# Optimization experiments

Measured on AMD Instinct MI355X. Metric: run time of the kernel, lower is better.

Reference implementation:

```python
import jax, jax.numpy as jnp
import numpy as np

DIM_IN, DIM_Q, DIM_K = 1024, 128, 128
B, S = 8, 2048

def setup_inputs() -> dict:
    key = jax.random.key(0)
    ks = jax.random.split(key, 9)
    sq = 1.0 / np.sqrt(DIM_IN)
    return {
        "query": jax.random.normal(ks[0], (B, S, DIM_IN), jnp.float32),
        "key": jax.random.normal(ks[1], (B, S, DIM_IN), jnp.float32),
        "value": jax.random.normal(ks[2], (B, S, DIM_IN), jnp.float32),
        "Wq": jax.random.uniform(ks[3], (DIM_IN, DIM_Q), jnp.float32, -sq, sq),
        "bq": jax.random.uniform(ks[4], (DIM_Q,), jnp.float32, -sq, sq),
        "Wk": jax.random.uniform(ks[5], (DIM_IN, DIM_K), jnp.float32, -sq, sq),
        "bk": jax.random.uniform(ks[6], (DIM_K,), jnp.float32, -sq, sq),
        "Wv": jax.random.uniform(ks[7], (DIM_IN, DIM_K), jnp.float32, -sq, sq),
        "bv": jax.random.uniform(ks[8], (DIM_K,), jnp.float32, -sq, sq),
    }

def reference(query, key, value, Wq, bq, Wk, bk, Wv, bv):
    q = jnp.einsum("bsd,dq->bsq", query, Wq) + bq          # [B,S,Dq]
    k = jnp.einsum("bsd,dk->bsk", key, Wk) + bk            # [B,S,Dk]
    v = jnp.einsum("bsd,dk->bsk", value, Wv) + bv          # [B,S,Dk]
    scale = jnp.asarray(q.shape[-1] ** 0.5, q.dtype)
    scores = jnp.einsum("bqd,bkd->bqk", q, k) / scale      # [B,S,S]
    attn = jax.nn.softmax(scores, axis=-1)
    return jnp.einsum("bqk,bkd->bqd", attn, v)             # [B,S,Dk]
```

## Files before the change

kernel.cpp:

```cpp
#include <hip/hip_runtime.h>

typedef __attribute__((ext_vector_type(8))) short short8;
typedef __attribute__((ext_vector_type(4))) float floatx4;

#define MFMA16(a, b, c) __builtin_amdgcn_mfma_f32_16x16x32_bf16(a, b, c, 0, 0, 0)

__device__ __forceinline__ short f2bf(float f) {
    unsigned int u = __float_as_uint(f);
    u = u + 0x7fffu + ((u >> 16) & 1u);
    return (short)(u >> 16);
}

__device__ __forceinline__ void ldst16(const void* g, void* l) {
    __builtin_amdgcn_global_load_lds(
        (const __attribute__((address_space(1))) void*)g,
        (__attribute__((address_space(3))) void*)l, 16, 0, 0);
}

__global__ __launch_bounds__(256) void wconv_kernel(const float* __restrict__ Wq,
                                                    const float* __restrict__ Wk,
                                                    const float* __restrict__ Wv,
                                                    short* __restrict__ wtf) {
    int idx = blockIdx.x * 256 + threadIdx.x;
    int w = idx >> 17;
    int rem = idx & 131071;
    int ks = rem >> 12;
    int r2 = rem & 4095;
    int nt = r2 >> 9;
    int r3 = r2 & 511;
    int lane = r3 >> 3, e = r3 & 7;
    int q4 = lane >> 4, l16 = lane & 15;
    int n = 16 * nt + l16;
    int k = 32 * ks + 8 * q4 + e;
    const float* W = (w == 0) ? Wq : (w == 1) ? Wk : Wv;
    wtf[idx] = f2bf(W[k * 128 + n]);
}

__global__ __launch_bounds__(256, 3) void proj_kernel(const float* __restrict__ Q,
                                                      const float* __restrict__ K,
                                                      const float* __restrict__ V,
                                                      const short* __restrict__ wtf,
                                                      const float* __restrict__ bq,
                                                      const float* __restrict__ bk,
                                                      const float* __restrict__ bv,
                                                      short* __restrict__ qo,
                                                      short* __restrict__ ko,
                                                      short* __restrict__ vo) {
    alignas(16) __shared__ float Asl[2][64 * 64];
    const int t = threadIdx.x;
    const int wv = t >> 6, L = t & 63;
    const int wm = wv >> 1, wn = wv & 1;
    const int q4 = L >> 4, l16 = L & 15;
    const int which = blockIdx.y;
    const float* A = (which == 0) ? Q : (which == 1) ? K : V;
    const short* Wf = wtf + which * 131072;
    const float* bias = (which == 0) ? bq : (which == 1) ? bk : bv;
    const int m0 = blockIdx.x * 64;

    floatx4 acc[2][4];
#pragma unroll
    for (int rg = 0; rg < 2; rg++)
#pragma unroll
        for (int nt = 0; nt < 4; nt++) acc[rg][nt] = (floatx4)0.0f;

    auto stage = [&](int buf, int k0) {
#pragma unroll
        for (int j = 0; j < 4; j++) {
            int s = j * 256 + t;
            int r = s >> 4, c = (s & 15) ^ (r & 15);
            ldst16(A + (size_t)(m0 + r) * 1024 + k0 + (c << 2),
                   &Asl[buf][(j * 256 + 64 * wv) * 4]);
        }
    };

    auto loadB = [&](int kc, short8 (&dst)[2][4]) {
#pragma unroll
        for (int ks = 0; ks < 2; ks++)
#pragma unroll
            for (int nt = 0; nt < 4; nt++)
                dst[ks][nt] = *(const short8*)(Wf +
                    (((size_t)(2 * kc + ks) * 8 + 4 * wn + nt) * 64 + L) * 8);
    };

    auto computeC = [&](int kc, short8 (&bfr)[2][4]) {
        short8 af[2][2];
#pragma unroll
        for (int rg = 0; rg < 2; rg++)
#pragma unroll
            for (int ks = 0; ks < 2; ks++) {
                int r = 32 * wm + 16 * rg + l16;
                int c0 = 8 * ks + 2 * q4;
                float4 f0 = *(float4*)&Asl[kc & 1][(r * 16 + (c0 ^ l16)) * 4];
                float4 f1 = *(float4*)&Asl[kc & 1][(r * 16 + ((c0 + 1) ^ l16)) * 4];
                short8 v;
                v[0] = f2bf(f0.x); v[1] = f2bf(f0.y); v[2] = f2bf(f0.z); v[3] = f2bf(f0.w);
                v[4] = f2bf(f1.x); v[5] = f2bf(f1.y); v[6] = f2bf(f1.z); v[7] = f2bf(f1.w);
                af[rg][ks] = v;
            }
        __builtin_amdgcn_s_setprio(1);
#pragma unroll
        for (int ks = 0; ks < 2; ks++)
#pragma unroll
            for (int nt = 0; nt < 4; nt++) {
                acc[0][nt] = MFMA16(af[0][ks], bfr[ks][nt], acc[0][nt]);
                acc[1][nt] = MFMA16(af[1][ks], bfr[ks][nt], acc[1][nt]);
            }
        __builtin_amdgcn_s_setprio(0);
    };

    short8 bA[2][4], bB[2][4];

#define PROJ_STEP(KC, BUSE, BLOAD)                                          \
    {                                                                       \
        if ((KC) + 1 < 16) {                                                \
            stage(((KC) + 1) & 1, ((KC) + 1) * 64);                         \
            loadB((KC) + 1, BLOAD);                                         \
            asm volatile("s_waitcnt vmcnt(12)" ::: "memory");               \
        } else {                                                            \
            asm volatile("s_waitcnt vmcnt(0)" ::: "memory");                \
        }                                                                   \
        __builtin_amdgcn_s_barrier();                                       \
        __builtin_amdgcn_sched_barrier(0);                                  \
        computeC((KC), BUSE);                                               \
        __builtin_amdgcn_sched_barrier(0);                                  \
        __builtin_amdgcn_s_barrier();                                       \
    }

    stage(0, 0);
    loadB(0, bA);

    for (int kc = 0; kc < 16; kc += 2) {
        PROJ_STEP(kc, bA, bB);
        PROJ_STEP(kc + 1, bB, bA);
    }
#undef PROJ_STEP

#pragma unroll
    for (int rg = 0; rg < 2; rg++) {
        const int rbase = m0 + 32 * wm + 16 * rg + q4 * 4;
#pragma unroll
        for (int nt = 0; nt < 4; nt++) {
            const int col = 64 * wn + 16 * nt + l16;
            float bvv = bias[col];
#pragma unroll
            for (int r = 0; r < 4; r++) {
                short h = f2bf(acc[rg][nt][r] + bvv);
                int grow = rbase + r;
                if (which == 0) {
                    qo[(size_t)grow * 128 + col] = h;
                } else if (which == 1) {
                    ko[(size_t)grow * 128 + col] = h;
                } else {
                    int bb = grow >> 11, s = grow & 2047;
                    vo[(size_t)bb * 262144 + (size_t)col * 2048 + s] = h;
                }
            }
        }
    }
}

__global__ __launch_bounds__(512, 2) void flash_kernel(const short* __restrict__ qw,
                                                       const short* __restrict__ kw,
                                                       const short* __restrict__ vw,
                                                       float* __restrict__ out) {
    alignas(16) __shared__ short Kls[2][2][64 * 128];
    alignas(16) __shared__ short Vls[2][2][128 * 64];
    alignas(16) __shared__ short Pl[2][64][72];
    const int t = threadIdx.x;
    const int wvi = t >> 6, L = t & 63;
    const int pr = wvi >> 2, wq = wvi & 3;
    const int pt = t & 255;
    const int q4 = L >> 4, l16 = L & 15;
    const int bid = blockIdx.x;
    const int b = bid & 7, bq = bid >> 3;
    const short* qp = qw + (size_t)b * 262144 + (size_t)bq * 64 * 128;
    const short* kp = kw + (size_t)b * 262144;
    const short* vp = vw + (size_t)b * 262144;

    short8 qf[4];
#pragma unroll
    for (int ks = 0; ks < 4; ks++)
        qf[ks] = *(const short8*)(qp + (16 * wq + l16) * 128 + ks * 32 + q4 * 8);

    floatx4 oacc[8];
#pragma unroll
    for (int dt = 0; dt < 8; dt++) oacc[dt] = (floatx4)0.0f;
    float ps[4] = {0.f, 0.f, 0.f, 0.f};
    const float SL = (float)(0.08838834764831845 * 1.4426950408889634);

    auto stage = [&](int buf, int kt) {
        const int kv0 = pr * 1024 + kt * 64;
#pragma unroll
        for (int j = 0; j < 4; j++) {
            int s = j * 256 + pt;
            int r = s >> 4, c = (s & 15) ^ (r & 15);
            ldst16(kp + (size_t)(kv0 + r) * 128 + c * 8,
                   &Kls[buf][pr][(j * 256 + 64 * wq) * 8]);
        }
#pragma unroll
        for (int j = 0; j < 4; j++) {
            int s = j * 256 + pt;
            int r = s >> 3, c = (s & 7) ^ (r & 7);
            ldst16(vp + (size_t)r * 2048 + kv0 + c * 8,
                   &Vls[buf][pr][(j * 256 + 64 * wq) * 8]);
        }
    };

    stage(0, 0);

    int cur = 0;
    for (int kt = 0; kt < 16; kt++) {
        if (kt + 1 < 16) {
            stage(cur ^ 1, kt + 1);
            asm volatile("s_waitcnt vmcnt(8)" ::: "memory");
        } else {
            asm volatile("s_waitcnt vmcnt(0)" ::: "memory");
        }
        __builtin_amdgcn_s_barrier();
        __builtin_amdgcn_sched_barrier(0);

        floatx4 sa[4];
        __builtin_amdgcn_s_setprio(1);
#pragma unroll
        for (int nt = 0; nt < 4; nt++) {
            sa[nt] = (floatx4)0.0f;
#pragma unroll
            for (int ks = 0; ks < 4; ks++) {
                short8 bfr = *(short8*)&Kls[cur][pr][(16 * nt + l16) * 128 + ((4 * ks + q4) ^ l16) * 8];
                sa[nt] = MFMA16(qf[ks], bfr, sa[nt]);
            }
        }
        __builtin_amdgcn_s_setprio(0);

#pragma unroll
        for (int nt = 0; nt < 4; nt++) {
#pragma unroll
            for (int r = 0; r < 4; r++) {
                float pv = __builtin_amdgcn_exp2f(sa[nt][r] * SL - 4.0f);
                ps[r] += pv;
                Pl[pr][16 * wq + q4 * 4 + r][16 * nt + l16] = f2bf(pv);
            }
        }

        short8 pf0 = *(short8*)&Pl[pr][16 * wq + l16][q4 * 8];
        short8 pf1 = *(short8*)&Pl[pr][16 * wq + l16][32 + q4 * 8];
        __builtin_amdgcn_s_setprio(1);
#pragma unroll
        for (int dt = 0; dt < 8; dt++) {
            short8 v0 = *(short8*)&Vls[cur][pr][(16 * dt + l16) * 64 + (q4 ^ (l16 & 7)) * 8];
            short8 v1 = *(short8*)&Vls[cur][pr][(16 * dt + l16) * 64 + ((4 + q4) ^ (l16 & 7)) * 8];
            oacc[dt] = MFMA16(pf0, v0, oacc[dt]);
            oacc[dt] = MFMA16(pf1, v1, oacc[dt]);
        }
        __builtin_amdgcn_s_setprio(0);

        __builtin_amdgcn_sched_barrier(0);
        __builtin_amdgcn_s_barrier();
        cur ^= 1;
    }

#pragma unroll
    for (int r = 0; r < 4; r++)
#pragma unroll
        for (int off = 1; off <= 8; off <<= 1)
            ps[r] += __shfl_xor(ps[r], off, 64);

    __syncthreads();
    float* Om = (float*)&Kls[0][0][0];
    float* Lm = (float*)&Vls[0][0][0];
    if (pr == 1) {
#pragma unroll
        for (int dt = 0; dt < 8; dt++)
#pragma unroll
            for (int r = 0; r < 4; r++)
                Om[(16 * wq + q4 * 4 + r) * 128 + 16 * dt + l16] = oacc[dt][r];
        if (l16 == 0)
#pragma unroll
            for (int r = 0; r < 4; r++)
                Lm[16 * wq + q4 * 4 + r] = ps[r];
    }
    __syncthreads();
    if (pr == 0) {
        float inv[4];
#pragma unroll
        for (int r = 0; r < 4; r++)
            inv[r] = 1.0f / (ps[r] + Lm[16 * wq + q4 * 4 + r]);
#pragma unroll
        for (int dt = 0; dt < 8; dt++) {
#pragma unroll
            for (int r = 0; r < 4; r++) {
                int row = 16 * wq + q4 * 4 + r;
                int qrow = bq * 64 + row;
                out[((size_t)b * 2048 + qrow) * 128 + 16 * dt + l16] =
                    (oacc[dt][r] + Om[row * 128 + 16 * dt + l16]) * inv[r];
            }
        }
    }
}

extern "C" void kernel_launch(void* const* d_in, const int* in_sizes, int n_in,
                              void* d_out, int out_size, void* d_ws, size_t ws_size,
                              hipStream_t stream) {
    const float* query = (const float*)d_in[0];
    const float* key   = (const float*)d_in[1];
    const float* value = (const float*)d_in[2];
    const float* Wq    = (const float*)d_in[3];
    const float* bq    = (const float*)d_in[4];
    const float* Wk    = (const float*)d_in[5];
    const float* bk    = (const float*)d_in[6];
    const float* Wv    = (const float*)d_in[7];
    const float* bv    = (const float*)d_in[8];
    float* out = (float*)d_out;

    short* wtf = (short*)d_ws;
    short* qws = wtf + 3 * 131072;
    short* kws = qws + 16384 * 128;
    short* vws = kws + 16384 * 128;

    wconv_kernel<<<1536, 256, 0, stream>>>(Wq, Wk, Wv, wtf);
    proj_kernel<<<dim3(256, 3), 256, 0, stream>>>(query, key, value, wtf,
                                                  bq, bk, bv, qws, kws, vws);
    flash_kernel<<<256, 512, 0, stream>>>(qws, kws, vws, out);
}
```

Measured before the change: 265.1 us.

## Replace direct global-to-LDS loads with register-staged prefetch in projection and flash kernels

Both the projection and flash-attention kernels stop using global_load_lds and instead load the next tile into registers, then write it to swizzled LDS after compute, so there is one barrier per iteration. The projection kernel is retiled to 32-row blocks with a 128-wide K step, doubling the grid and giving each wave a 32-column slice. Launch-bound occupancy hints are loosened. The changes trade the asynchronous DMA path for extra VGPRs and explicit LDS writes, which may lower occupancy or expose global load latency.

```diff
diff --git a/kernel.cpp b/kernel.cpp
--- a/kernel.cpp
+++ b/kernel.cpp
@@ -9,12 +9,6 @@
     unsigned int u = __float_as_uint(f);
     u = u + 0x7fffu + ((u >> 16) & 1u);
     return (short)(u >> 16);
-}
-
-__device__ __forceinline__ void ldst16(const void* g, void* l) {
-    __builtin_amdgcn_global_load_lds(
-        (const __attribute__((address_space(1))) void*)g,
-        (__attribute__((address_space(3))) void*)l, 16, 0, 0);
 }
 
 __global__ __launch_bounds__(256) void wconv_kernel(const float* __restrict__ Wq,
@@ -36,7 +30,7 @@
     wtf[idx] = f2bf(W[k * 128 + n]);
 }
 
-__global__ __launch_bounds__(256, 3) void proj_kernel(const float* __restrict__ Q,
+__global__ __launch_bounds__(256, 2) void proj_kernel(const float* __restrict__ Q,
                                                       const float* __restrict__ K,
                                                       const float* __restrict__ V,
                                                       const short* __restrict__ wtf,
@@ -46,101 +40,107 @@
                                                       short* __restrict__ qo,
                                                       short* __restrict__ ko,
                                                       short* __restrict__ vo) {
-    alignas(16) __shared__ float Asl[2][64 * 64];
+    alignas(16) __shared__ float Asl[2][32 * 128];
     const int t = threadIdx.x;
     const int wv = t >> 6, L = t & 63;
-    const int wm = wv >> 1, wn = wv & 1;
+    const int wn = wv;
     const int q4 = L >> 4, l16 = L & 15;
     const int which = blockIdx.y;
     const float* A = (which == 0) ? Q : (which == 1) ? K : V;
     const short* Wf = wtf + which * 131072;
     const float* bias = (which == 0) ? bq : (which == 1) ? bk : bv;
-    const int m0 = blockIdx.x * 64;
-
-    floatx4 acc[2][4];
+    const int m0 = blockIdx.x * 32;
+
+    floatx4 acc[2][2];
 #pragma unroll
     for (int rg = 0; rg < 2; rg++)
 #pragma unroll
-        for (int nt = 0; nt < 4; nt++) acc[rg][nt] = (floatx4)0.0f;
-
-    auto stage = [&](int buf, int k0) {
-#pragma unroll
-        for (int j = 0; j < 4; j++) {
-            int s = j * 256 + t;
-            int r = s >> 4, c = (s & 15) ^ (r & 15);
-            ldst16(A + (size_t)(m0 + r) * 1024 + k0 + (c << 2),
-                   &Asl[buf][(j * 256 + 64 * wv) * 4]);
-        }
-    };
-
-    auto loadB = [&](int kc, short8 (&dst)[2][4]) {
-#pragma unroll
-        for (int ks = 0; ks < 2; ks++)
-#pragma unroll
-            for (int nt = 0; nt < 4; nt++)
-                dst[ks][nt] = *(const short8*)(Wf +
-                    (((size_t)(2 * kc + ks) * 8 + 4 * wn + nt) * 64 + L) * 8);
-    };
-
-    auto computeC = [&](int kc, short8 (&bfr)[2][4]) {
-        short8 af[2][2];
-#pragma unroll
-        for (int rg = 0; rg < 2; rg++)
-#pragma unroll
-            for (int ks = 0; ks < 2; ks++) {
-                int r = 32 * wm + 16 * rg + l16;
+        for (int nt = 0; nt < 2; nt++) acc[rg][nt] = (floatx4)0.0f;
+
+    float4 arA[4], arB[4];
+    short8 bfr[4][2];
+
+    auto loadA = [&](int k0, float4 (&ar)[4]) {
+#pragma unroll
+        for (int j = 0; j < 4; j++) {
+            int s = j * 256 + t, r = s >> 5, c = s & 31;
+            ar[j] = *(const float4*)(A + (size_t)(m0 + r) * 1024 + k0 + c * 4);
+        }
+    };
+    auto writeA = [&](int buf, float4 (&ar)[4]) {
+#pragma unroll
+        for (int j = 0; j < 4; j++) {
+            int s = j * 256 + t, r = s >> 5, c = s & 31;
+            *(float4*)&Asl[buf][(r * 32 + (c ^ (r & 15))) * 4] = ar[j];
+        }
+    };
+    auto loadB = [&](int kc) {
+#pragma unroll
+        for (int ks = 0; ks < 4; ks++)
+#pragma unroll
+            for (int nt = 0; nt < 2; nt++)
+                bfr[ks][nt] = *(const short8*)(Wf +
+                    (((size_t)(4 * kc + ks) * 8 + 2 * wn + nt) * 64 + L) * 8);
+    };
+    auto computeC = [&](int kc) {
+#pragma unroll
+        for (int ks = 0; ks < 4; ks++) {
+            short8 af[2];
+#pragma unroll
+            for (int rg = 0; rg < 2; rg++) {
+                int r = 16 * rg + l16;
                 int c0 = 8 * ks + 2 * q4;
-                float4 f0 = *(float4*)&Asl[kc & 1][(r * 16 + (c0 ^ l16)) * 4];
-                float4 f1 = *(float4*)&Asl[kc & 1][(r * 16 + ((c0 + 1) ^ l16)) * 4];
+                float4 f0 = *(float4*)&Asl[kc & 1][(r * 32 + (c0 ^ l16)) * 4];
+                float4 f1 = *(float4*)&Asl[kc & 1][(r * 32 + ((c0 + 1) ^ l16)) * 4];
                 short8 v;
                 v[0] = f2bf(f0.x); v[1] = f2bf(f0.y); v[2] = f2bf(f0.z); v[3] = f2bf(f0.w);
                 v[4] = f2bf(f1.x); v[5] = f2bf(f1.y); v[6] = f2bf(f1.z); v[7] = f2bf(f1.w);
-                af[rg][ks] = v;
-            }
-        __builtin_amdgcn_s_setprio(1);
-#pragma unroll
-        for (int ks = 0; ks < 2; ks++)
-#pragma unroll
-            for (int nt = 0; nt < 4; nt++) {
-                acc[0][nt] = MFMA16(af[0][ks], bfr[ks][nt], acc[0][nt]);
-                acc[1][nt] = MFMA16(af[1][ks], bfr[ks][nt], acc[1][nt]);
-            }
-        __builtin_amdgcn_s_setprio(0);
-    };
-
-    short8 bA[2][4], bB[2][4];
-
-#define PROJ_STEP(KC, BUSE, BLOAD)                                          \
+                af[rg] = v;
+            }
+            __builtin_amdgcn_s_setprio(1);
+#pragma unroll
+            for (int nt = 0; nt < 2; nt++) {
+                acc[0][nt] = MFMA16(af[0], bfr[ks][nt], acc[0][nt]);
+                acc[1][nt] = MFMA16(af[1], bfr[ks][nt], acc[1][nt]);
+            }
+            __builtin_amdgcn_s_setprio(0);
+        }
+    };
+
+#define PROJ_STEP(KC, LDBANK, WRBANK)                                       \
     {                                                                       \
-        if ((KC) + 1 < 16) {                                                \
-            stage(((KC) + 1) & 1, ((KC) + 1) * 64);                         \
-            loadB((KC) + 1, BLOAD);                                         \
-            asm volatile("s_waitcnt vmcnt(12)" ::: "memory");               \
-        } else {                                                            \
-            asm volatile("s_waitcnt vmcnt(0)" ::: "memory");                \
+        if ((KC) + 2 < 8) loadA(((KC) + 2) * 128, LDBANK);                  \
+        __builtin_amdgcn_sched_barrier(0);                                  \
+        computeC(KC);                                                       \
+        if ((KC) + 1 < 8) {                                                 \
+            loadB((KC) + 1);                                                \
+            writeA(((KC) + 1) & 1, WRBANK);        \
         }                                                                   \
-        __builtin_amdgcn_s_barrier();                                       \
-        __builtin_amdgcn_sched_barrier(0);                                  \
-        computeC((KC), BUSE);                                               \
+        asm volatile("s_waitcnt lgkmcnt(0)" ::: "memory");                  \
         __builtin_amdgcn_sched_barrier(0);                                  \
         __builtin_amdgcn_s_barrier();                                       \
     }
 
-    stage(0, 0);
-    loadB(0, bA);
-
-    for (int kc = 0; kc < 16; kc += 2) {
-        PROJ_STEP(kc, bA, bB);
-        PROJ_STEP(kc + 1, bB, bA);
+    loadA(0, arA);
+    loadA(128, arB);
+    loadB(0);
+    writeA(0, arA);
+    asm volatile("s_waitcnt lgkmcnt(0)" ::: "memory");
+    __builtin_amdgcn_sched_barrier(0);
+    __builtin_amdgcn_s_barrier();
+
+    for (int kc = 0; kc < 8; kc += 2) {
+        PROJ_STEP(kc, arA, arB);
+        PROJ_STEP(kc + 1, arB, arA);
     }
 #undef PROJ_STEP
 
 #pragma unroll
     for (int rg = 0; rg < 2; rg++) {
-        const int rbase = m0 + 32 * wm + 16 * rg + q4 * 4;
-#pragma unroll
-        for (int nt = 0; nt < 4; nt++) {
-            const int col = 64 * wn + 16 * nt + l16;
+        const int rbase = m0 + 16 * rg + q4 * 4;
+#pragma unroll
+        for (int nt = 0; nt < 2; nt++) {
+            const int col = 32 * wn + 16 * nt + l16;
             float bvv = bias[col];
 #pragma unroll
             for (int r = 0; r < 4; r++) {
@@ -159,10 +159,10 @@
     }
 }
 
-__global__ __launch_bounds__(512, 2) void flash_kernel(const short* __restrict__ qw,
-                                                       const short* __restrict__ kw,
-                                                       const short* __restrict__ vw,
-                                                       float* __restrict__ out) {
+__global__ __launch_bounds__(512) void flash_kernel(const short* __restrict__ qw,
+                                                    const short* __restrict__ kw,
+                                                    const short* __restrict__ vw,
+                                                    float* __restrict__ out) {
     alignas(16) __shared__ short Kls[2][2][64 * 128];
     alignas(16) __shared__ short Vls[2][2][128 * 64];
     alignas(16) __shared__ short Pl[2][64][72];
@@ -188,35 +188,43 @@
     float ps[4] = {0.f, 0.f, 0.f, 0.f};
     const float SL = (float)(0.08838834764831845 * 1.4426950408889634);
 
-    auto stage = [&](int buf, int kt) {
+    short8 kreg[4], vreg[4];
+
+    auto loadKV = [&](int kt) {
         const int kv0 = pr * 1024 + kt * 64;
 #pragma unroll
         for (int j = 0; j < 4; j++) {
-            int s = j * 256 + pt;
-            int r = s >> 4, c = (s & 15) ^ (r & 15);
-            ldst16(kp + (size_t)(kv0 + r) * 128 + c * 8,
-                   &Kls[buf][pr][(j * 256 + 64 * wq) * 8]);
-        }
-#pragma unroll
-        for (int j = 0; j < 4; j++) {
-            int s = j * 256 + pt;
-            int r = s >> 3, c = (s & 7) ^ (r & 7);
-            ldst16(vp + (size_t)r * 2048 + kv0 + c * 8,
-                   &Vls[buf][pr][(j * 256 + 64 * wq) * 8]);
-        }
-    };
-
-    stage(0, 0);
-
-    int cur = 0;
+            int s = j * 256 + pt, r = s >> 4, c = s & 15;
+            kreg[j] = *(const short8*)(kp + (size_t)(kv0 + r) * 128 + c * 8);
+        }
+#pragma unroll
+        for (int j = 0; j < 4; j++) {
+            int s = j * 256 + pt, r = s >> 3, c = s & 7;
+            vreg[j] = *(const short8*)(vp + (size_t)r * 2048 + kv0 + c * 8);
+        }
+    };
+    auto writeKV = [&](int buf) {
+#pragma unroll
+        for (int j = 0; j < 4; j++) {
+            int s = j * 256 + pt, r = s >> 4, c = s & 15;
+            *(short8*)&Kls[buf][pr][(r * 16 + (c ^ (r & 15))) * 8] = kreg[j];
+        }
+#pragma unroll
+        for (int j = 0; j < 4; j++) {
+            int s = j * 256 + pt, r = s >> 3, c = s & 7;
+            *(short8*)&Vls[buf][pr][(r * 8 + (c ^ (r & 7))) * 8] = vreg[j];
+        }
+    };
+
+    loadKV(0);
+    writeKV(0);
+    asm volatile("s_waitcnt lgkmcnt(0)" ::: "memory");
+    __builtin_amdgcn_sched_barrier(0);
+    __builtin_amdgcn_s_barrier();
+
     for (int kt = 0; kt < 16; kt++) {
-        if (kt + 1 < 16) {
-            stage(cur ^ 1, kt + 1);
-            asm volatile("s_waitcnt vmcnt(8)" ::: "memory");
-        } else {
-            asm volatile("s_waitcnt vmcnt(0)" ::: "memory");
-        }
-        __builtin_amdgcn_s_barrier();
+        const int cur = kt & 1;
+        if (kt + 1 < 16) loadKV(kt + 1);
         __builtin_amdgcn_sched_barrier(0);
 
         floatx4 sa[4];
@@ -254,9 +262,10 @@
         }
         __builtin_amdgcn_s_setprio(0);
 
+        if (kt + 1 < 16) writeKV(cur ^ 1);
+        asm volatile("s_waitcnt lgkmcnt(0)" ::: "memory");
         __builtin_amdgcn_sched_barrier(0);
         __builtin_amdgcn_s_barrier();
-        cur ^= 1;
     }
 
 #pragma unroll
@@ -318,7 +327,7 @@
     short* vws = kws + 16384 * 128;
 
     wconv_kernel<<<1536, 256, 0, stream>>>(Wq, Wk, Wv, wtf);
-    proj_kernel<<<dim3(256, 3), 256, 0, stream>>>(query, key, value, wtf,
+    proj_kernel<<<dim3(512, 3), 256, 0, stream>>>(query, key, value, wtf,
                                                   bq, bk, bv, qws, kws, vws);
     flash_kernel<<<256, 512, 0, stream>>>(qws, kws, vws, out);
 }
```

Result: slower. 290.6 us (+9.6%).
